# Kernel tuning notes

Measured on AMD Instinct MI355X. Metric: run time of the kernel, lower is better.

The kernel has to match this reference:

```python
import jax, jax.numpy as jnp
import numpy as np

HEAD = 8  # number of attention heads (init kwarg)


def setup_inputs() -> dict:
    key = jax.random.key(0)
    k1, k2, k3 = jax.random.split(key, 3)
    b, H, W, c = 8, 32, 32, 512
    dim = 512
    x = jax.random.normal(k1, (b, H, W, c), dtype=jnp.float32)
    # 1x1 Conv == per-pixel matmul over channels
    w_qkv = jax.random.normal(k2, (c, 3 * dim), dtype=jnp.float32) * (c ** -0.5)
    w_out = jax.random.normal(k3, (dim, dim), dtype=jnp.float32) * (dim ** -0.5)
    b_out = jnp.zeros((dim,), dtype=jnp.float32)
    return {"x": x, "w_qkv": w_qkv, "w_out": w_out, "b_out": b_out}


def reference(x, w_qkv, w_out, b_out):
    b, H, W, c = x.shape
    n = H * W
    # QKV 1x1-conv projection (no bias)
    qkv = jnp.einsum('bhwc,cd->bhwd', x, w_qkv)          # (b, H, W, 3*dim)
    qkv = qkv.reshape(b, n, HEAD, -1)                     # (b, n, head, 3*dh)
    q, k, v = jnp.split(qkv, 3, axis=-1)                  # each (b, n, head, dh)
    scale = b ** -0.5  # NOTE: source scales by batch size, reproduced faithfully
    attn = jax.nn.softmax(jnp.einsum('bihd,bjhd->bhij', q, k) * scale, axis=-1)
    out = jnp.einsum('bhij,bjhd->bihd', attn, v)          # (b, n, head, dh)
    out = out.reshape(b, H, W, -1)                        # (b, H, W, dim)
    # output 1x1-conv projection (with bias)
    return jnp.einsum('bhwc,cd->bhwd', out, w_out) + b_out
```

## Files before the change

### kernel.cpp

```cpp
#include <hip/hip_runtime.h>
#include <hip/hip_bf16.h>

typedef __bf16 bf16x8_t  __attribute__((ext_vector_type(8)));
typedef float  f32x4_t   __attribute__((ext_vector_type(4)));
typedef float  f32x16_t  __attribute__((ext_vector_type(16)));
typedef short  s16x4_t   __attribute__((ext_vector_type(4)));
typedef short  s16x8_t   __attribute__((ext_vector_type(8)));

#define NTOK   1024
#define CDIM   512
#define QKVDIM 1536
#define NHEAD  8
#define DHEAD  64
#define C1EXP  0.51007088f
#define C2EXP  34.624681f

__device__ __forceinline__ float b2f(short s) {
    unsigned int u = ((unsigned int)(unsigned short)s) << 16;
    float f; __builtin_memcpy(&f, &u, 4); return f;
}
__device__ __forceinline__ short f2b(float f) {
    __bf16 h = (__bf16)f; short s; __builtin_memcpy(&s, &h, 2); return s;
}

__global__ __launch_bounds__(256) void cvt_fused(
    const float* __restrict__ x, const float* __restrict__ wq,
    const float* __restrict__ wo, short* __restrict__ xb,
    short* __restrict__ wqbT, short* __restrict__ wobT)
{
    int bid = blockIdx.x;
    if (bid < 2048) {
        int i = bid * 256 + threadIdx.x;
        const float* p = x + (size_t)i * 8;
        float4 a = *(const float4*)p, b = *(const float4*)(p + 4);
        s16x8_t v;
        v[0]=f2b(a.x); v[1]=f2b(a.y); v[2]=f2b(a.z); v[3]=f2b(a.w);
        v[4]=f2b(b.x); v[5]=f2b(b.y); v[6]=f2b(b.z); v[7]=f2b(b.w);
        *(s16x8_t*)(xb + (size_t)i * 8) = v;
    } else if (bid < 5120) {
        int i = (bid - 2048) * 256 + threadIdx.x;
        int k = i / QKVDIM, n = i % QKVDIM;
        wqbT[(size_t)n * 512 + k] = f2b(wq[i]);
    } else {
        int i = (bid - 5120) * 256 + threadIdx.x;
        int k = i >> 9, n = i & 511;
        wobT[(size_t)n * 512 + k] = f2b(wo[i]);
    }
}

__global__ __launch_bounds__(256) void gemm_qkv(
    const short* __restrict__ A, const short* __restrict__ Bt,
    short* __restrict__ qk, short* __restrict__ vT)
{
    __shared__ __align__(16) short Al[128 * 64];
    __shared__ __align__(16) short Bl[128 * 64];

    const int t = threadIdx.x;
    const int g = blockIdx.x;
    const int N0 = (g >> 6) * 128, M0 = (g & 63) * 128;
    const int w = t >> 6, lane = t & 63;
    const int q5 = lane & 31, hi = lane >> 5;
    const int wm = (w >> 1) * 64, wn = (w & 1) * 64;

    int srow[4], soff[4];
#pragma unroll
    for (int r = 0; r < 4; ++r) {
        int ci = r * 256 + t;
        srow[r] = ci >> 3;
        soff[r] = (ci & 7) * 8;
    }
    const short* Ag = A  + (size_t)M0 * 512;
    const short* Bg = Bt + (size_t)N0 * 512;

    s16x8_t ar[4], br[4];
#pragma unroll
    for (int r = 0; r < 4; ++r) {
        ar[r] = *(const s16x8_t*)(Ag + (size_t)srow[r] * 512 + soff[r]);
        br[r] = *(const s16x8_t*)(Bg + (size_t)srow[r] * 512 + soff[r]);
    }

    f32x16_t acc[2][2];
#pragma unroll
    for (int mt = 0; mt < 2; ++mt)
#pragma unroll
        for (int nt = 0; nt < 2; ++nt)
#pragma unroll
            for (int r = 0; r < 16; ++r) acc[mt][nt][r] = 0.f;

#pragma unroll 1
    for (int kc = 0; kc < 8; ++kc) {
        __syncthreads();
#pragma unroll
        for (int r = 0; r < 4; ++r) {
            int lds = srow[r] * 64 + (((soff[r] >> 3) ^ (srow[r] & 7)) * 8);
            *(s16x8_t*)(Al + lds) = ar[r];
            *(s16x8_t*)(Bl + lds) = br[r];
        }
        __syncthreads();
        if (kc < 7) {
            int k0 = (kc + 1) * 64;
#pragma unroll
            for (int r = 0; r < 4; ++r) {
                ar[r] = *(const s16x8_t*)(Ag + (size_t)srow[r] * 512 + k0 + soff[r]);
                br[r] = *(const s16x8_t*)(Bg + (size_t)srow[r] * 512 + k0 + soff[r]);
            }
        }
#pragma unroll
        for (int c = 0; c < 4; ++c) {
            bf16x8_t af[2], bf[2];
#pragma unroll
            for (int mt = 0; mt < 2; ++mt) {
                int rr = wm + mt * 32 + q5;
                af[mt] = *(const bf16x8_t*)(Al + rr * 64 + (((2 * c + hi) ^ (rr & 7)) * 8));
            }
#pragma unroll
            for (int nt = 0; nt < 2; ++nt) {
                int rr = wn + nt * 32 + q5;
                bf[nt] = *(const bf16x8_t*)(Bl + rr * 64 + (((2 * c + hi) ^ (rr & 7)) * 8));
            }
#pragma unroll
            for (int mt = 0; mt < 2; ++mt)
#pragma unroll
                for (int nt = 0; nt < 2; ++nt)
                    acc[mt][nt] = __builtin_amdgcn_mfma_f32_32x32x16_bf16(
                        af[mt], bf[nt], acc[mt][nt], 0, 0, 0);
        }
    }

#pragma unroll
    for (int mt = 0; mt < 2; ++mt) {
#pragma unroll
        for (int nt = 0; nt < 2; ++nt) {
            int c0 = N0 + wn + nt * 32;
            int hh = c0 / 192, r0 = c0 % 192;
            if (r0 < 128) {
#pragma unroll
                for (int r = 0; r < 16; ++r) {
                    int row = M0 + wm + mt * 32 + (r & 3) + 8 * (r >> 2) + 4 * hi;
                    qk[(size_t)row * 1024 + hh * 128 + r0 + q5] = f2b(acc[mt][nt][r]);
                }
            } else {
#pragma unroll
                for (int rg = 0; rg < 4; ++rg) {
                    int row4 = M0 + wm + mt * 32 + 8 * rg + 4 * hi;
                    int bb = row4 >> 10, ti = row4 & 1023;
                    s16x4_t v4;
#pragma unroll
                    for (int i = 0; i < 4; ++i) v4[i] = f2b(acc[mt][nt][rg * 4 + i]);
                    *(s16x4_t*)(vT + ((size_t)(bb * 8 + hh) * 64 + (r0 - 128) + q5) * 1024 + ti) = v4;
                }
            }
        }
    }
}

template <int N, bool BIAS>
__global__ __launch_bounds__(256) void gemm128(
    const short* __restrict__ A, const short* __restrict__ Bt,
    const float* __restrict__ bias, float* __restrict__ C)
{
    __shared__ __align__(16) short Al[128 * 64];
    __shared__ __align__(16) short Bl[128 * 64];

    const int t = threadIdx.x;
    const int g = blockIdx.x;
    const int N0 = (g >> 6) * 128, M0 = (g & 63) * 128;
    const int w = t >> 6, lane = t & 63;
    const int q5 = lane & 31, hi = lane >> 5;
    const int wm = (w >> 1) * 64, wn = (w & 1) * 64;

    int srow[4], soff[4];
#pragma unroll
    for (int r = 0; r < 4; ++r) {
        int ci = r * 256 + t;
        srow[r] = ci >> 3;
        soff[r] = (ci & 7) * 8;
    }
    const short* Ag = A  + (size_t)M0 * 512;
    const short* Bg = Bt + (size_t)N0 * 512;

    s16x8_t ar[4], br[4];
#pragma unroll
    for (int r = 0; r < 4; ++r) {
        ar[r] = *(const s16x8_t*)(Ag + (size_t)srow[r] * 512 + soff[r]);
        br[r] = *(const s16x8_t*)(Bg + (size_t)srow[r] * 512 + soff[r]);
    }

    f32x16_t acc[2][2];
#pragma unroll
    for (int mt = 0; mt < 2; ++mt)
#pragma unroll
        for (int nt = 0; nt < 2; ++nt)
#pragma unroll
            for (int r = 0; r < 16; ++r) acc[mt][nt][r] = 0.f;

#pragma unroll 1
    for (int kc = 0; kc < 8; ++kc) {
        __syncthreads();
#pragma unroll
        for (int r = 0; r < 4; ++r) {
            int lds = srow[r] * 64 + (((soff[r] >> 3) ^ (srow[r] & 7)) * 8);
            *(s16x8_t*)(Al + lds) = ar[r];
            *(s16x8_t*)(Bl + lds) = br[r];
        }
        __syncthreads();
        if (kc < 7) {
            int k0 = (kc + 1) * 64;
#pragma unroll
            for (int r = 0; r < 4; ++r) {
                ar[r] = *(const s16x8_t*)(Ag + (size_t)srow[r] * 512 + k0 + soff[r]);
                br[r] = *(const s16x8_t*)(Bg + (size_t)srow[r] * 512 + k0 + soff[r]);
            }
        }
#pragma unroll
        for (int c = 0; c < 4; ++c) {
            bf16x8_t af[2], bf[2];
#pragma unroll
            for (int mt = 0; mt < 2; ++mt) {
                int rr = wm + mt * 32 + q5;
                af[mt] = *(const bf16x8_t*)(Al + rr * 64 + (((2 * c + hi) ^ (rr & 7)) * 8));
            }
#pragma unroll
            for (int nt = 0; nt < 2; ++nt) {
                int rr = wn + nt * 32 + q5;
                bf[nt] = *(const bf16x8_t*)(Bl + rr * 64 + (((2 * c + hi) ^ (rr & 7)) * 8));
            }
#pragma unroll
            for (int mt = 0; mt < 2; ++mt)
#pragma unroll
                for (int nt = 0; nt < 2; ++nt)
                    acc[mt][nt] = __builtin_amdgcn_mfma_f32_32x32x16_bf16(
                        af[mt], bf[nt], acc[mt][nt], 0, 0, 0);
        }
    }

#pragma unroll
    for (int mt = 0; mt < 2; ++mt)
#pragma unroll
        for (int nt = 0; nt < 2; ++nt) {
            int col = N0 + wn + nt * 32 + q5;
            float bz = BIAS ? bias[col] : 0.f;
#pragma unroll
            for (int r = 0; r < 16; ++r) {
                int row = M0 + wm + mt * 32 + (r & 3) + 8 * (r >> 2) + 4 * hi;
                C[(size_t)row * N + col] = acc[mt][nt][r] + bz;
            }
        }
}

__global__ __launch_bounds__(256) void attn32(
    const short* __restrict__ qk, const short* __restrict__ vT,
    short* __restrict__ aout)
{
    __shared__ __align__(16) short Kl[64 * 72];
    __shared__ __align__(16) short Vt[64 * 72];
    __shared__ __align__(16) short Pl[4][32 * 72];
    __shared__ float Ls[4][32];

    const int t = threadIdx.x;
    const int g = blockIdx.x;
    const int qb = (g >> 3) & 7;
    const int bh = ((g >> 6) << 3) | (g & 7);
    const int h = bh & 7, b = bh >> 3;
    const int w = t >> 6, lane = t & 63;
    const int q5 = lane & 31, hi = lane >> 5;
    const int key = (lane >> 3) & 3;

    const size_t qrow = (size_t)(b * NTOK + qb * 128 + w * 32 + q5) * 1024
                        + h * 128 + hi * 8;
    bf16x8_t qf[4];
#pragma unroll
    for (int c = 0; c < 4; ++c) qf[c] = *(const bf16x8_t*)(qk + qrow + 16 * c);

    float lsum = 0.f;
    f32x16_t O[2];
#pragma unroll
    for (int dt = 0; dt < 2; ++dt)
#pragma unroll
        for (int r = 0; r < 16; ++r) O[dt][r] = 0.f;

    short* Pm = Pl[w];

    const int r0i = t >> 3, r1i = r0i + 32, c8 = (t & 7) * 8;
    const int soff = ((t & 7) ^ w) * 8;
    const size_t kgbase = (size_t)(b * NTOK) * 1024 + h * 128 + 64 + c8;
    const size_t vgbase = (size_t)(b * 8 + h) * 64 * 1024 + c8;

    s16x8_t k0r, k1r, v0r, v1r;
    k0r = *(const s16x8_t*)(qk + kgbase + (size_t)r0i * 1024);
    k1r = *(const s16x8_t*)(qk + kgbase + (size_t)r1i * 1024);
    v0r = *(const s16x8_t*)(vT + vgbase + (size_t)r0i * 1024);
    v1r = *(const s16x8_t*)(vT + vgbase + (size_t)r1i * 1024);

#pragma unroll 1
    for (int jt = 0; jt < 16; ++jt) {
        *(s16x8_t*)(Kl + r0i * 72 + soff) = k0r;
        *(s16x8_t*)(Kl + r1i * 72 + soff) = k1r;
        *(s16x8_t*)(Vt + r0i * 72 + soff) = v0r;
        *(s16x8_t*)(Vt + r1i * 72 + soff) = v1r;
        __syncthreads();

        if (jt < 15) {
            int j0n = (jt + 1) * 64;
            k0r = *(const s16x8_t*)(qk + kgbase + (size_t)(j0n + r0i) * 1024);
            k1r = *(const s16x8_t*)(qk + kgbase + (size_t)(j0n + r1i) * 1024);
            v0r = *(const s16x8_t*)(vT + vgbase + (size_t)r0i * 1024 + j0n);
            v1r = *(const s16x8_t*)(vT + vgbase + (size_t)r1i * 1024 + j0n);
        }

#pragma unroll
        for (int jb = 0; jb < 2; ++jb) {
            f32x16_t s;
#pragma unroll
            for (int r = 0; r < 16; ++r) s[r] = 0.f;
#pragma unroll
            for (int c = 0; c < 4; ++c) {
                int phys = (2 * c + hi) ^ key;
                bf16x8_t kf = *(const bf16x8_t*)(Kl + (jb * 32 + q5) * 72 + phys * 8);
                s = __builtin_amdgcn_mfma_f32_32x32x16_bf16(kf, qf[c], s, 0, 0, 0);
            }
#pragma unroll
            for (int g2 = 0; g2 < 4; ++g2) {
                s16x4_t pv;
#pragma unroll
                for (int i = 0; i < 4; ++i) {
                    short hh = f2b(__builtin_amdgcn_exp2f(s[g2 * 4 + i] * C1EXP - C2EXP));
                    pv[i] = hh;
                    lsum += b2f(hh);
                }
                int phys = ((jb * 4 + g2) ^ key);
                *(s16x4_t*)(Pm + q5 * 72 + phys * 8 + 4 * hi) = pv;
            }
        }

        bf16x8_t pa[4];
#pragma unroll
        for (int c = 0; c < 4; ++c) {
            int phys = (2 * c + hi) ^ key;
            pa[c] = *(const bf16x8_t*)(Pm + q5 * 72 + phys * 8);
        }

#pragma unroll
        for (int dt = 0; dt < 2; ++dt)
#pragma unroll
            for (int c = 0; c < 4; ++c) {
                int phys = (2 * c + hi) ^ key;
                bf16x8_t vf = *(const bf16x8_t*)(Vt + (dt * 32 + q5) * 72 + phys * 8);
                O[dt] = __builtin_amdgcn_mfma_f32_32x32x16_bf16(pa[c], vf, O[dt], 0, 0, 0);
            }
        __syncthreads();
    }

    lsum += __shfl_xor(lsum, 32, 64);
    if (lane < 32) Ls[w][lane] = lsum;
#pragma unroll
    for (int dt = 0; dt < 2; ++dt)
#pragma unroll
        for (int r = 0; r < 16; ++r) {
            int qloc = (r & 3) + 8 * (r >> 2) + 4 * hi;
            float inv = 1.f / Ls[w][qloc];
            size_t tok = (size_t)(b * NTOK + qb * 128 + w * 32 + qloc);
            aout[tok * CDIM + h * DHEAD + dt * 32 + q5] = f2b(O[dt][r] * inv);
        }
}

extern "C" void kernel_launch(void* const* d_in, const int* in_sizes, int n_in,
                              void* d_out, int out_size, void* d_ws, size_t ws_size,
                              hipStream_t stream)
{
    const float* x     = (const float*)d_in[0];
    const float* w_qkv = (const float*)d_in[1];
    const float* w_out = (const float*)d_in[2];
    const float* b_out = (const float*)d_in[3];
    for (int i = 0; i < n_in; ++i) {
        if      (in_sizes[i] == 4194304) x     = (const float*)d_in[i];
        else if (in_sizes[i] ==  786432) w_qkv = (const float*)d_in[i];
        else if (in_sizes[i] ==  262144) w_out = (const float*)d_in[i];
        else if (in_sizes[i] ==     512) b_out = (const float*)d_in[i];
    }

    short* qk   = (short*)d_ws;
    short* vT   = (short*)((char*)d_ws + (size_t)8192 * 1024 * 2);
    short* aout = (short*)((char*)d_ws + (size_t)8192 * 1024 * 2 + (size_t)64 * 64 * 1024 * 2);
    short* wobT = (short*)((char*)d_ws + (size_t)33 * 1024 * 1024 + (size_t)1664 * 1024);
    short* xb   = (short*)d_out;
    short* wqbT = (short*)d_out + (size_t)8192 * 512;

    cvt_fused<<<6144, 256, 0, stream>>>(x, w_qkv, w_out, xb, wqbT, wobT);

    gemm_qkv<<<768, 256, 0, stream>>>(xb, wqbT, qk, vT);

    attn32<<<512, 256, 0, stream>>>(qk, vT, aout);

    gemm128<CDIM, true><<<256, 256, 0, stream>>>(aout, wobT, b_out, (float*)d_out);
}
```

Before: 148.9 us.

## Merge all stages into one cooperative persistent kernel with grid syncs

Combines the conversion, QKV GEMM, attention and output GEMM into a single cooperative kernel of 512 blocks, with grid-wide syncs between stages. The goal is to remove the launch gaps and tail drain between the four separate kernels. In exchange, shared memory is the union of every stage's buffers and occupancy is fixed at 2 blocks per CU. Stages whose tile count does not match 512 either loop unevenly or leave blocks idle. The old four-kernel path is kept as a fallback if the cooperative launch fails.

```diff
diff --git a/kernel.cpp b/kernel.cpp
--- a/kernel.cpp
+++ b/kernel.cpp
@@ -1,8 +1,10 @@
 #include <hip/hip_runtime.h>
 #include <hip/hip_bf16.h>
+#include <hip/hip_cooperative_groups.h>
+
+namespace cg = cooperative_groups;
 
 typedef __bf16 bf16x8_t  __attribute__((ext_vector_type(8)));
-typedef float  f32x4_t   __attribute__((ext_vector_type(4)));
 typedef float  f32x16_t  __attribute__((ext_vector_type(16)));
 typedef short  s16x4_t   __attribute__((ext_vector_type(4)));
 typedef short  s16x8_t   __attribute__((ext_vector_type(8)));
@@ -10,8 +12,6 @@
 #define NTOK   1024
 #define CDIM   512
 #define QKVDIM 1536
-#define NHEAD  8
-#define DHEAD  64
 #define C1EXP  0.51007088f
 #define C2EXP  34.624681f
 
@@ -23,12 +23,11 @@
     __bf16 h = (__bf16)f; short s; __builtin_memcpy(&s, &h, 2); return s;
 }
 
-__global__ __launch_bounds__(256) void cvt_fused(
-    const float* __restrict__ x, const float* __restrict__ wq,
+__device__ __forceinline__ void cvt_body(
+    int bid, const float* __restrict__ x, const float* __restrict__ wq,
     const float* __restrict__ wo, short* __restrict__ xb,
     short* __restrict__ wqbT, short* __restrict__ wobT)
 {
-    int bid = blockIdx.x;
     if (bid < 2048) {
         int i = bid * 256 + threadIdx.x;
         const float* p = x + (size_t)i * 8;
@@ -48,15 +47,12 @@
     }
 }
 
-__global__ __launch_bounds__(256) void gemm_qkv(
-    const short* __restrict__ A, const short* __restrict__ Bt,
-    short* __restrict__ qk, short* __restrict__ vT)
-{
-    __shared__ __align__(16) short Al[128 * 64];
-    __shared__ __align__(16) short Bl[128 * 64];
-
+__device__ __forceinline__ void gemm_qkv_tile(
+    int g, const short* __restrict__ A, const short* __restrict__ Bt,
+    short* __restrict__ qk, short* __restrict__ vT,
+    short* __restrict__ Al, short* __restrict__ Bl)
+{
     const int t = threadIdx.x;
-    const int g = blockIdx.x;
     const int N0 = (g >> 6) * 128, M0 = (g & 63) * 128;
     const int w = t >> 6, lane = t & 63;
     const int q5 = lane & 31, hi = lane >> 5;
@@ -154,16 +150,13 @@
     }
 }
 
-template <int N, bool BIAS>
-__global__ __launch_bounds__(256) void gemm128(
-    const short* __restrict__ A, const short* __restrict__ Bt,
-    const float* __restrict__ bias, float* __restrict__ C)
-{
-    __shared__ __align__(16) short Al[128 * 64];
-    __shared__ __align__(16) short Bl[128 * 64];
-
+__device__ __forceinline__ void gemm128_tile(
+    int g, const short* __restrict__ A, const short* __restrict__ Bt,
+    const float* __restrict__ bias, float* __restrict__ C,
+    short* __restrict__ Al, short* __restrict__ Bl)
+{
+    constexpr int N = CDIM;
     const int t = threadIdx.x;
-    const int g = blockIdx.x;
     const int N0 = (g >> 6) * 128, M0 = (g & 63) * 128;
     const int w = t >> 6, lane = t & 63;
     const int q5 = lane & 31, hi = lane >> 5;
@@ -239,7 +232,7 @@
 #pragma unroll
         for (int nt = 0; nt < 2; ++nt) {
             int col = N0 + wn + nt * 32 + q5;
-            float bz = BIAS ? bias[col] : 0.f;
+            float bz = bias[col];
 #pragma unroll
             for (int r = 0; r < 16; ++r) {
                 int row = M0 + wm + mt * 32 + (r & 3) + 8 * (r >> 2) + 4 * hi;
@@ -248,17 +241,12 @@
         }
 }
 
-__global__ __launch_bounds__(256) void attn32(
-    const short* __restrict__ qk, const short* __restrict__ vT,
-    short* __restrict__ aout)
-{
-    __shared__ __align__(16) short Kl[64 * 72];
-    __shared__ __align__(16) short Vt[64 * 72];
-    __shared__ __align__(16) short Pl[4][32 * 72];
-    __shared__ float Ls[4][32];
-
+__device__ __forceinline__ void attn_tile(
+    int g, const short* __restrict__ qk, const short* __restrict__ vT,
+    short* __restrict__ aout, short* __restrict__ Kl, short* __restrict__ Vt,
+    short* __restrict__ Pl, float* __restrict__ Ls)
+{
     const int t = threadIdx.x;
-    const int g = blockIdx.x;
     const int qb = (g >> 3) & 7;
     const int bh = ((g >> 6) << 3) | (g & 7);
     const int h = bh & 7, b = bh >> 3;
@@ -279,7 +267,7 @@
 #pragma unroll
         for (int r = 0; r < 16; ++r) O[dt][r] = 0.f;
 
-    short* Pm = Pl[w];
+    short* Pm = Pl + w * (32 * 72);
 
     const int r0i = t >> 3, r1i = r0i + 32, c8 = (t & 7) * 8;
     const int soff = ((t & 7) ^ w) * 8;
@@ -352,16 +340,77 @@
     }
 
     lsum += __shfl_xor(lsum, 32, 64);
-    if (lane < 32) Ls[w][lane] = lsum;
+    if (lane < 32) Ls[w * 32 + lane] = lsum;
 #pragma unroll
     for (int dt = 0; dt < 2; ++dt)
 #pragma unroll
         for (int r = 0; r < 16; ++r) {
             int qloc = (r & 3) + 8 * (r >> 2) + 4 * hi;
-            float inv = 1.f / Ls[w][qloc];
+            float inv = 1.f / Ls[w * 32 + qloc];
             size_t tok = (size_t)(b * NTOK + qb * 128 + w * 32 + qloc);
-            aout[tok * CDIM + h * DHEAD + dt * 32 + q5] = f2b(O[dt][r] * inv);
-        }
+            aout[tok * CDIM + h * 64 + dt * 32 + q5] = f2b(O[dt][r] * inv);
+        }
+}
+
+__global__ __launch_bounds__(256, 2) void mega(
+    const float* __restrict__ x, const float* __restrict__ wq,
+    const float* __restrict__ wo, const float* __restrict__ bias,
+    short* __restrict__ xb, short* __restrict__ wqbT, short* __restrict__ wobT,
+    short* __restrict__ qk, short* __restrict__ vT, short* __restrict__ aout,
+    float* __restrict__ out)
+{
+    __shared__ __align__(16) short Al[128 * 64];
+    __shared__ __align__(16) short Bl[128 * 64];
+    __shared__ __align__(16) short Kl[64 * 72];
+    __shared__ __align__(16) short Vt[64 * 72];
+    __shared__ __align__(16) short Pl[4 * 32 * 72];
+    __shared__ float Ls[4 * 32];
+
+    cg::grid_group grid = cg::this_grid();
+
+    for (int vb = blockIdx.x; vb < 6144; vb += 512)
+        cvt_body(vb, x, wq, wo, xb, wqbT, wobT);
+    grid.sync();
+
+    for (int g = blockIdx.x; g < 768; g += 512)
+        gemm_qkv_tile(g, xb, wqbT, qk, vT, Al, Bl);
+    grid.sync();
+
+    attn_tile(blockIdx.x, qk, vT, aout, Kl, Vt, Pl, Ls);
+    grid.sync();
+
+    for (int g = blockIdx.x; g < 256; g += 512)
+        gemm128_tile(g, aout, wobT, bias, out, Al, Bl);
+}
+
+__global__ __launch_bounds__(256) void k_cvt(
+    const float* x, const float* wq, const float* wo,
+    short* xb, short* wqbT, short* wobT)
+{
+    cvt_body(blockIdx.x, x, wq, wo, xb, wqbT, wobT);
+}
+__global__ __launch_bounds__(256) void k_gemm_qkv(
+    const short* A, const short* Bt, short* qk, short* vT)
+{
+    __shared__ __align__(16) short Al[128 * 64];
+    __shared__ __align__(16) short Bl[128 * 64];
+    gemm_qkv_tile(blockIdx.x, A, Bt, qk, vT, Al, Bl);
+}
+__global__ __launch_bounds__(256) void k_attn(
+    const short* qk, const short* vT, short* aout)
+{
+    __shared__ __align__(16) short Kl[64 * 72];
+    __shared__ __align__(16) short Vt[64 * 72];
+    __shared__ __align__(16) short Pl[4 * 32 * 72];
+    __shared__ float Ls[4 * 32];
+    attn_tile(blockIdx.x, qk, vT, aout, Kl, Vt, Pl, Ls);
+}
+__global__ __launch_bounds__(256) void k_gemm128(
+    const short* A, const short* Bt, const float* bias, float* C)
+{
+    __shared__ __align__(16) short Al[128 * 64];
+    __shared__ __align__(16) short Bl[128 * 64];
+    gemm128_tile(blockIdx.x, A, Bt, bias, C, Al, Bl);
 }
 
 extern "C" void kernel_launch(void* const* d_in, const int* in_sizes, int n_in,
@@ -385,12 +434,20 @@
     short* wobT = (short*)((char*)d_ws + (size_t)33 * 1024 * 1024 + (size_t)1664 * 1024);
     short* xb   = (short*)d_out;
     short* wqbT = (short*)d_out + (size_t)8192 * 512;
-
-    cvt_fused<<<6144, 256, 0, stream>>>(x, w_qkv, w_out, xb, wqbT, wobT);
-
-    gemm_qkv<<<768, 256, 0, stream>>>(xb, wqbT, qk, vT);
-
-    attn32<<<512, 256, 0, stream>>>(qk, vT, aout);
-
-    gemm128<CDIM, true><<<256, 256, 0, stream>>>(aout, wobT, b_out, (float*)d_out);
-}
+    float* outp = (float*)d_out;
+
+    void* args[] = {
+        (void*)&x, (void*)&w_qkv, (void*)&w_out, (void*)&b_out,
+        (void*)&xb, (void*)&wqbT, (void*)&wobT,
+        (void*)&qk, (void*)&vT, (void*)&aout, (void*)&outp
+    };
+    hipError_t err = hipLaunchCooperativeKernel(
+        (const void*)mega, dim3(512), dim3(256), args, 0, stream);
+
+    if (err != hipSuccess) {
+        k_cvt<<<6144, 256, 0, stream>>>(x, w_qkv, w_out, xb, wqbT, wobT);
+        k_gemm_qkv<<<768, 256, 0, stream>>>(xb, wqbT, qk, vT);
+        k_attn<<<512, 256, 0, stream>>>(qk, vT, aout);
+        k_gemm128<<<256, 256, 0, stream>>>(aout, wobT, b_out, outp);
+    }
+}
```

After: 346.4 us. +132.6%, slower.
